# Kernel tuning notes

Hardware: AMD Instinct MI355X
Metric: run time of the kernel (lower is better)

Reference implementation:

```python
import jax, jax.numpy as jnp
import numpy as np


def _gru_dirs(x, h, w_ih, w_hh, b_ih, b_hh):
    # One GRU step for both directions at once (seq_len==1 per original loop).
    # x: [N, in], h: [2, N, H]; w_ih: [2, 3H, in], w_hh: [2, 3H, H], biases [2, 3H]
    gi = jnp.einsum('ni,dgi->dng', x, w_ih) + b_ih[:, None, :]
    gh = jnp.einsum('dnh,dgh->dng', h, w_hh) + b_hh[:, None, :]
    H = h.shape[-1]
    ir, iz, inn = gi[..., :H], gi[..., H:2 * H], gi[..., 2 * H:]
    hr, hz, hn = gh[..., :H], gh[..., H:2 * H], gh[..., 2 * H:]
    r = jax.nn.sigmoid(ir + hr)
    z = jax.nn.sigmoid(iz + hz)
    n = jnp.tanh(inn + r * hn)
    return (1.0 - z) * n + z * h


def setup_inputs() -> dict:
    key = jax.random.key(0)
    ks = jax.random.split(key, 6)
    V, E, H, NL = 32000, 1024, 512, 2  # vocab, input_size, hidden_size, num_layers
    N, L = 32, 512
    s = 0.05
    x = jax.random.randint(ks[0], (N, L), 0, V)
    emb = jax.random.normal(ks[1], (V, E), dtype=jnp.float32) * s
    w_ih = jax.random.normal(ks[2], (NL, 2, 3 * H, E), dtype=jnp.float32) * s
    w_hh = jax.random.normal(ks[3], (NL, 2, 3 * H, H), dtype=jnp.float32) * s
    b_ih = jax.random.normal(ks[4], (NL, 2, 3 * H), dtype=jnp.float32) * s
    b_hh = jax.random.normal(ks[5], (NL, 2, 3 * H), dtype=jnp.float32) * s
    return {"x": x, "emb": emb, "w_ih": w_ih, "w_hh": w_hh, "b_ih": b_ih, "b_hh": b_hh}


def reference(x, emb, w_ih, w_hh, b_ih, b_hh):
    # Because the torch code calls the bidirectional GRU one timestep at a time
    # with a carried hidden, BOTH directions scan left-to-right over the sequence.
    N, L = x.shape
    num_layers = w_ih.shape[0]
    H = w_hh.shape[-1]
    h0 = jnp.zeros((num_layers, 2, N, H), dtype=emb.dtype)

    def step(h, xt):
        layer_in = emb[xt]  # [N, E] embedding lookup for this timestep
        new_h = []
        for l in range(num_layers):  # fixed small layer loop
            hl = _gru_dirs(layer_in, h[l], w_ih[l], w_hh[l], b_ih[l], b_hh[l])
            new_h.append(hl)
            layer_in = jnp.concatenate([hl[0], hl[1]], axis=-1)  # [N, 2H]
        hs = jnp.stack(new_h)  # [num_layers, 2, N, H]
        return hs, (layer_in, hs)

    _, (outs, hiddens) = jax.lax.scan(step, h0, x.T)  # scan over L timesteps
    outputs = jnp.transpose(outs, (1, 0, 2))  # [N, L, 2H]
    hiddens = hiddens.reshape(L, num_layers * 2, N, H)  # [L, 2*num_layers, N, H]
    return outputs, hiddens
```

## Files before the change

### kernel.cpp

```cpp
#include <hip/hip_runtime.h>
#include <hip/hip_bf16.h>

using u16 = unsigned short;
using u32 = unsigned int;
using bf16x8 = __attribute__((ext_vector_type(8))) __bf16;
using f32x4  = __attribute__((ext_vector_type(4))) float;
using u32x4  = __attribute__((ext_vector_type(4))) u32;

#define GLP(p) ((const __attribute__((address_space(1))) void*)(p))
#define LDSP(p) ((__attribute__((address_space(3))) void*)(p))

__device__ __forceinline__ float bf2f(u16 u) {
    union { float f; u32 i; } v; v.i = ((u32)u) << 16; return v.f;
}
__device__ __forceinline__ u16 f2bf(float f) {
    union { float f; u32 i; } v; v.f = f;
    u32 r = v.i + 0x7FFFu + ((v.i >> 16) & 1u);
    return (u16)(r >> 16);
}

__device__ __forceinline__ u32 ld_sc01_u32(const u32* p) {
    u32 v;
    asm volatile("global_load_dword %0, %1, off sc0 sc1\n\ts_waitcnt vmcnt(0)"
                 : "=v"(v) : "v"(p) : "memory");
    return v;
}
__device__ __forceinline__ void st_sc01_u32(u32* p, u32 v) {
    asm volatile("global_store_dword %0, %1, off sc0 sc1" :: "v"(p), "v"(v) : "memory");
}
__device__ __forceinline__ void st_sc01_u16(u16* p, u16 v) {
    asm volatile("global_store_short %0, %1, off sc0 sc1" :: "v"(p), "v"(v) : "memory");
}
__device__ __forceinline__ void st_sc01_u32x4(u16* p, u32x4 v) {
    asm volatile("global_store_dwordx4 %0, %1, off sc0 sc1" :: "v"(p), "v"(v) : "memory");
}

__device__ __forceinline__ float sigm(float x) {
    return __builtin_amdgcn_rcpf(1.f + __expf(-x));
}
__device__ __forceinline__ float tanh_fast(float x) {
    float e = __expf(-2.f * x);
    return (1.f - e) * __builtin_amdgcn_rcpf(1.f + e);
}

__global__ void k_gather(const int* __restrict__ x, const float* __restrict__ emb,
                         u16* __restrict__ X0) {
    int gid = blockIdx.x * blockDim.x + threadIdx.x;
    if (gid >= 16384 * 256) return;
    int e4 = gid << 2;
    int m = e4 >> 10, k = e4 & 1023;
    int t = m >> 5, n = m & 31;
    int tok = x[n * 512 + t];
    float4 v = *reinterpret_cast<const float4*>(emb + ((size_t)tok << 10) + k);
    ushort4 o;
    o.x = f2bf(v.x); o.y = f2bf(v.y); o.z = f2bf(v.z); o.w = f2bf(v.w);
    *reinterpret_cast<ushort4*>(X0 + (size_t)e4) = o;
}

__global__ void k_f32bf16(const float* __restrict__ s, u16* __restrict__ d, int n4) {
    int gid = blockIdx.x * blockDim.x + threadIdx.x;
    if (gid >= n4) return;
    float4 v = reinterpret_cast<const float4*>(s)[gid];
    ushort4 o;
    o.x = f2bf(v.x); o.y = f2bf(v.y); o.z = f2bf(v.z); o.w = f2bf(v.w);
    reinterpret_cast<ushort4*>(d)[gid] = o;
}

template<int LAYER>
__device__ __forceinline__ void gru_body(char* smem, int d, int wg,
    const u16* __restrict__ Gi, const u16* __restrict__ Whh_l,
    const float* __restrict__ bhh_l, u16* __restrict__ hbuf,
    u16* __restrict__ X1, float* __restrict__ hid, float* __restrict__ outp,
    u32* __restrict__ flags, u32* __restrict__ xflags, const u32* __restrict__ gdone)
{
    char* hS          = smem;
    float (*ghs)[196] = (float(*)[196])(smem + 32768);
    u16 (*gis)[208]   = (u16(*)[208])(smem + 57856);
    float* bhh_s      = (float*)(smem + 71168);
    u16* hvS          = (u16*)(smem + 71936);
    volatile u32* rdy = (volatile u32*)(smem + 76032);
    const int tid = threadIdx.x;
    const int lane = tid & 63, w = tid >> 6;
    const int j0 = wg * 64;
    const int g = w >> 2;
    const int lr = lane & 15, lk = lane >> 4;

    if (tid < 192) {
        int g2 = tid >> 6, jj = tid & 63;
        bhh_s[tid] = bhh_l[d * 1536 + g2 * 512 + j0 + jj];
    }
    if (tid < 8) rdy[tid] = 0;
    bf16x8 wf[16];
    {
        const int joff = (w & 3) * 16;
        const u16* wr = Whh_l + (size_t)(d * 1536 + g * 512 + j0 + joff + lr) * 512 + lk * 8;
        #pragma unroll
        for (int kt = 0; kt < 16; ++kt)
            wf[kt] = *reinterpret_cast<const bf16x8*>(wr + kt * 32);
    }
    __syncthreads();

    u32* myflag = flags + (d * 8 + wg) * 32;
    const u32* wflag = flags + (d * 8 + (w & 7)) * 32;

    const int c8 = (lane & 7) * 8;
    const int rb = lane >> 3;
    const int colu = w * 64 + c8;
    const int ci0 = (tid - 512) * 3;

    float hpv[4] = {0.f, 0.f, 0.f, 0.f};
    u32 g_seen = 0;

    for (int t = 0; t < 512; ++t) {
        if (w < 8) {
            if (t > 0) {
                long long tt0 = __builtin_amdgcn_s_memrealtime();
                int k = 0;
                while (ld_sc01_u32(wflag) < (u32)t) {
                    if (++k >= 16) {
                        k = 0;
                        if (__builtin_amdgcn_s_memrealtime() - tt0 > 2000) {
                            if (lane == 0)
                                __hip_atomic_store(myflag, (u32)t, __ATOMIC_RELEASE,
                                                   __HIP_MEMORY_SCOPE_AGENT);
                            tt0 = __builtin_amdgcn_s_memrealtime();
                        }
                    }
                }
            }
            const u16* hb = hbuf + ((size_t)d * 2 + ((t + 1) & 1)) * 16384;
            u32x4 v0, v1, v2, v3;
            asm volatile("global_load_dwordx4 %0, %1, off sc0 sc1"
                         : "=v"(v0) : "v"(hb + (size_t)(rb)      * 512 + colu));
            asm volatile("global_load_dwordx4 %0, %1, off sc0 sc1"
                         : "=v"(v1) : "v"(hb + (size_t)(rb + 8)  * 512 + colu));
            asm volatile("global_load_dwordx4 %0, %1, off sc0 sc1"
                         : "=v"(v2) : "v"(hb + (size_t)(rb + 16) * 512 + colu));
            asm volatile("global_load_dwordx4 %0, %1, off sc0 sc1"
                         : "=v"(v3) : "v"(hb + (size_t)(rb + 24) * 512 + colu));
            asm volatile("s_waitcnt vmcnt(0)" ::: "memory");
            const int cb = colu * 2;
            *reinterpret_cast<u32x4*>(hS + (rb)      * 1024 + (cb ^ (((rb)      & 15) << 4))) = v0;
            *reinterpret_cast<u32x4*>(hS + (rb + 8)  * 1024 + (cb ^ (((rb + 8)  & 15) << 4))) = v1;
            *reinterpret_cast<u32x4*>(hS + (rb + 16) * 1024 + (cb ^ (((rb + 16) & 15) << 4))) = v2;
            *reinterpret_cast<u32x4*>(hS + (rb + 24) * 1024 + (cb ^ (((rb + 24) & 15) << 4))) = v3;
            asm volatile("s_waitcnt lgkmcnt(0)" ::: "memory");
            __builtin_amdgcn_sched_barrier(0);
            if (lane == 0) rdy[w] = (u32)(t + 1);
        } else {
            u32 yneed = (u32)(t >> 2);
            if (g_seen <= yneed) {
                const u32* gp = gdone + yneed;
                long long T0 = __builtin_amdgcn_s_memrealtime();
                while (ld_sc01_u32(gp) == 0) {
                    __builtin_amdgcn_s_sleep(1);
                    if (__builtin_amdgcn_s_memrealtime() - T0 > 2000000) break;
                }
                g_seen = yneed + 1;
            }
            u32x4 gq[3];
            int nbs[3], gcs[3];
            #pragma unroll
            for (int i = 0; i < 3; ++i) {
                int ci = ci0 + i;
                nbs[i] = ci / 24; gcs[i] = ci % 24;
                const u16* gp = Gi + (size_t)(t * 32 + nbs[i]) * 3072 + d * 1536
                              + (gcs[i] >> 3) * 512 + j0 + (gcs[i] & 7) * 8;
                asm volatile("global_load_dwordx4 %0, %1, off sc0 sc1"
                             : "=v"(gq[i]) : "v"(gp));
            }
            asm volatile("s_waitcnt vmcnt(0)" ::: "memory");
            #pragma unroll
            for (int i = 0; i < 3; ++i)
                *reinterpret_cast<u32x4*>(&gis[nbs[i]][gcs[i] * 8]) = gq[i];
        }

        f32x4 acc0 = {0.f, 0.f, 0.f, 0.f}, acc1 = acc0;
        #pragma unroll
        for (int s = 0; s < 8; ++s) {
            while (rdy[s] < (u32)(t + 1)) {}
            __builtin_amdgcn_sched_barrier(0);
            int b0 = (lk * 16 + (2 * s) * 64) ^ (lr << 4);
            int b1 = (lk * 16 + (2 * s + 1) * 64) ^ (lr << 4);
            bf16x8 a00 = *reinterpret_cast<const bf16x8*>(hS + lr * 1024 + b0);
            bf16x8 a10 = *reinterpret_cast<const bf16x8*>(hS + (16 + lr) * 1024 + b0);
            bf16x8 a01 = *reinterpret_cast<const bf16x8*>(hS + lr * 1024 + b1);
            bf16x8 a11 = *reinterpret_cast<const bf16x8*>(hS + (16 + lr) * 1024 + b1);
            acc0 = __builtin_amdgcn_mfma_f32_16x16x32_bf16(a00, wf[2 * s],     acc0, 0, 0, 0);
            acc1 = __builtin_amdgcn_mfma_f32_16x16x32_bf16(a10, wf[2 * s],     acc1, 0, 0, 0);
            acc0 = __builtin_amdgcn_mfma_f32_16x16x32_bf16(a01, wf[2 * s + 1], acc0, 0, 0, 0);
            acc1 = __builtin_amdgcn_mfma_f32_16x16x32_bf16(a11, wf[2 * s + 1], acc1, 0, 0, 0);
        }
        int colg = w * 16 + lr;
        float bv = bhh_s[colg];
        #pragma unroll
        for (int q = 0; q < 4; ++q) {
            ghs[lk * 4 + q][colg]      = acc0[q] + bv;
            ghs[16 + lk * 4 + q][colg] = acc1[q] + bv;
        }
        __syncthreads();

        u16* hbw = hbuf + ((size_t)d * 2 + (t & 1)) * 16384;
        #pragma unroll
        for (int rep = 0; rep < 2; ++rep) {
            int e2 = tid + rep * 768;
            if (e2 < 1024) {
                int jp = (e2 & 31) * 2, nb = e2 >> 5;
                float r0 = sigm(bf2f(gis[nb][jp])      + ghs[nb][jp]);
                float r1 = sigm(bf2f(gis[nb][jp + 1])  + ghs[nb][jp + 1]);
                float z0 = sigm(bf2f(gis[nb][64 + jp])     + ghs[nb][64 + jp]);
                float z1 = sigm(bf2f(gis[nb][64 + jp + 1]) + ghs[nb][64 + jp + 1]);
                float n0 = tanh_fast(bf2f(gis[nb][128 + jp])     + r0 * ghs[nb][128 + jp]);
                float n1 = tanh_fast(bf2f(gis[nb][128 + jp + 1]) + r1 * ghs[nb][128 + jp + 1]);
                float hv0 = (1.f - z0) * n0 + z0 * hpv[rep * 2];
                float hv1 = (1.f - z1) * n1 + z1 * hpv[rep * 2 + 1];
                hpv[rep * 2] = hv0; hpv[rep * 2 + 1] = hv1;
                u32 packed = (u32)f2bf(hv0) | ((u32)f2bf(hv1) << 16);
                st_sc01_u32((u32*)(hbw + (size_t)nb * 512 + j0 + jp), packed);
                *reinterpret_cast<u32*>(hvS + nb * 64 + jp) = packed;
            }
        }
        asm volatile("s_waitcnt vmcnt(0)" ::: "memory");
        __syncthreads();
        if (tid == 16)
            st_sc01_u32(myflag, (u32)(t + 1));

        if (tid >= 512) {
            int q = tid - 512, nb = q >> 3, j8 = (q & 7) * 8;
            union { u32x4 v; u16 s[8]; } h8;
            h8.v = *reinterpret_cast<const u32x4*>(hvS + nb * 64 + j8);
            float f0 = bf2f(h8.s[0]), f1 = bf2f(h8.s[1]), f2 = bf2f(h8.s[2]), f3 = bf2f(h8.s[3]);
            float f4 = bf2f(h8.s[4]), f5 = bf2f(h8.s[5]), f6 = bf2f(h8.s[6]), f7 = bf2f(h8.s[7]);
            float* hp = hid + ((size_t)(t * 4 + LAYER * 2 + d) * 32 + nb) * 512 + j0 + j8;
            *reinterpret_cast<float4*>(hp)     = make_float4(f0, f1, f2, f3);
            *reinterpret_cast<float4*>(hp + 4) = make_float4(f4, f5, f6, f7);
            if (LAYER == 0) {
                u16* xp = X1 + (size_t)(t * 32 + nb) * 1024 + (size_t)d * 512 + j0 + j8;
                st_sc01_u32x4(xp, h8.v);
            } else {
                float* op = outp + ((size_t)nb * 512 + t) * 1024 + (size_t)d * 512 + j0 + j8;
                *reinterpret_cast<float4*>(op)     = make_float4(f0, f1, f2, f3);
                *reinterpret_cast<float4*>(op + 4) = make_float4(f4, f5, f6, f7);
            }
        }
        if (LAYER == 0 && (t & 3) == 3) {
            asm volatile("s_waitcnt vmcnt(0)" ::: "memory");
            __syncthreads();
            if (tid == 17)
                st_sc01_u32(xflags + (d * 8 + wg) * 32, (u32)(t + 1));
        }
    }
}

__device__ __forceinline__ void chaser_body(char* smem, int cw,
    const u16* __restrict__ A, const u16* __restrict__ B,
    const float* __restrict__ bias, u16* __restrict__ Gi,
    const u32* __restrict__ xflags, u32* __restrict__ cnt, u32* __restrict__ done)
{
    u16* As = (u16*)smem;
    u16* Bs = (u16*)(smem + 16384);
    const int tid = threadIdx.x;
    const int lane = tid & 63, wid = tid >> 6;
    const int wm = wid & 1, wn = wid >> 1;
    const int lr = lane & 15, lk = lane >> 4;

    for (int T = cw; T < 4096; T += 48) {
        const int y = T >> 5, x = T & 31;
        if (xflags && tid < 16) {
            const u32* fp = xflags + tid * 32;
            u32 target = 4u * (u32)y + 4u;
            long long T0 = __builtin_amdgcn_s_memrealtime();
            while (ld_sc01_u32(fp) < target) {
                __builtin_amdgcn_s_sleep(4);
                if (__builtin_amdgcn_s_memrealtime() - T0 > 2000000) break;
            }
        }
        __syncthreads();

        f32x4 zero = {0.f, 0.f, 0.f, 0.f};
        f32x4 acc[4][2];
        #pragma unroll
        for (int i = 0; i < 4; ++i) { acc[i][0] = zero; acc[i][1] = zero; }

        for (int k0 = 0; k0 < 1024; k0 += 64) {
            #pragma unroll
            for (int r = 0; r < 5; ++r) {
                int c = wid * 5 + r;
                if (c < 16) {
                    int o = c * 1024 + lane * 16;
                    int row = o >> 7, kb = o & 127;
                    int kbs = kb ^ ((row & 7) << 4);
                    const char* s = (const char*)A + ((size_t)(y * 128 + row) * 1024 + k0) * 2 + kbs;
                    __builtin_amdgcn_global_load_lds(GLP(s), LDSP((char*)As + c * 1024), 16, 0, 0);
                } else if (c < 28) {
                    int c2 = c - 16;
                    int o = c2 * 1024 + lane * 16;
                    int row = o >> 7, kb = o & 127;
                    int kbs = kb ^ ((row & 7) << 4);
                    const char* s = (const char*)B + ((size_t)(x * 96 + row) * 1024 + k0) * 2 + kbs;
                    __builtin_amdgcn_global_load_lds(GLP(s), LDSP((char*)Bs + c2 * 1024), 16, 0, 0);
                }
            }
            __syncthreads();
            if (wid < 6) {
                #pragma unroll
                for (int kk = 0; kk < 2; ++kk) {
                    bf16x8 af[4], bfr[2];
                    int kb = kk * 64 + lk * 16;
                    #pragma unroll
                    for (int i = 0; i < 4; ++i) {
                        int rowA = wm * 64 + i * 16 + lr;
                        af[i] = *reinterpret_cast<const bf16x8*>((const char*)As + rowA * 128 + (kb ^ ((rowA & 7) << 4)));
                    }
                    #pragma unroll
                    for (int j = 0; j < 2; ++j) {
                        int rowB = wn * 32 + j * 16 + lr;
                        bfr[j] = *reinterpret_cast<const bf16x8*>((const char*)Bs + rowB * 128 + (kb ^ ((rowB & 7) << 4)));
                    }
                    #pragma unroll
                    for (int i = 0; i < 4; ++i)
                        #pragma unroll
                        for (int j = 0; j < 2; ++j)
                            acc[i][j] = __builtin_amdgcn_mfma_f32_16x16x32_bf16(af[i], bfr[j], acc[i][j], 0, 0, 0);
                }
            }
            __syncthreads();
        }
        if (wid < 6) {
            #pragma unroll
            for (int j = 0; j < 2; ++j) {
                int col = x * 96 + wn * 32 + j * 16 + lr;
                float bv = bias[col];
                #pragma unroll
                for (int i = 0; i < 4; ++i) {
                    int rowb = y * 128 + wm * 64 + i * 16 + lk * 4;
                    #pragma unroll
                    for (int q = 0; q < 4; ++q)
                        st_sc01_u16(Gi + (size_t)(rowb + q) * 3072 + col, f2bf(acc[i][j][q] + bv));
                }
            }
        }
        asm volatile("s_waitcnt vmcnt(0)" ::: "memory");
        __syncthreads();
        if (tid == 0) {
            u32 old = __hip_atomic_fetch_add(&cnt[y], 1u, __ATOMIC_RELAXED,
                                             __HIP_MEMORY_SCOPE_AGENT);
            if (old == 31u)
                st_sc01_u32((u32*)&done[y], 1u);
        }
    }
}

__global__ __launch_bounds__(768, 2) void k_fused(
    u16* __restrict__ Gi,
    const u16* __restrict__ X0, const u16* __restrict__ Wih,
    const float* __restrict__ b_ih,
    const u16* __restrict__ Whh, const float* __restrict__ bhh,
    u16* __restrict__ hbuf0, u16* __restrict__ hbuf1,
    u16* __restrict__ X1,
    float* __restrict__ hid, float* __restrict__ outp,
    u32* __restrict__ flags0, u32* __restrict__ flags1,
    u32* __restrict__ xflags,
    u32* __restrict__ g0cnt, u32* __restrict__ g0done,
    u32* __restrict__ g1cnt, u32* __restrict__ g1done)
{
    __shared__ __align__(16) char smem[76096];
    int bid = blockIdx.x;
    if (bid < 16) {
        gru_body<0>(smem, bid >> 3, bid & 7, Gi, Whh, bhh, hbuf0,
                    X1, hid, outp, flags0, xflags, g0done);
    } else if (bid < 64) {
        chaser_body(smem, bid - 16, X0, Wih, b_ih, Gi, nullptr, g0cnt, g0done);
    } else if (bid < 112) {
        chaser_body(smem, bid - 64, X1, Wih + (size_t)3072 * 1024, b_ih + 3072,
                    Gi, xflags, g1cnt, g1done);
    } else {
        int b = bid - 112;
        gru_body<1>(smem, b >> 3, b & 7, Gi, Whh + (size_t)3072 * 512, bhh + 3072,
                    hbuf1, nullptr, hid, outp, flags1, nullptr, g1done);
    }
}

extern "C" void kernel_launch(void* const* d_in, const int* in_sizes, int n_in,
                              void* d_out, int out_size, void* d_ws, size_t ws_size,
                              hipStream_t stream) {
    const int*   x    = (const int*)d_in[0];
    const float* emb  = (const float*)d_in[1];
    const float* w_ih = (const float*)d_in[2];
    const float* w_hh = (const float*)d_in[3];
    const float* b_ih = (const float*)d_in[4];
    const float* b_hh = (const float*)d_in[5];
    float* outp = (float*)d_out;
    float* hid  = outp + (size_t)32 * 512 * 1024;

    char* ws = (char*)d_ws;
    u16* X0     = (u16*)(ws);
    u16* X1     = (u16*)(ws + 33554432);
    u16* Wih    = (u16*)(ws + 67108864);
    u16* Whh    = (u16*)(ws + 79691776);
    u16* Gi     = (u16*)(ws + 85983232);
    u16* hbuf0  = (u16*)(ws + 186646528);
    u16* hbuf1  = (u16*)(ws + 186777600);
    u32* flags0 = (u32*)(ws + 186908672);
    u32* flags1 = (u32*)(ws + 186910720);
    u32* xflags = (u32*)(ws + 186912768);
    u32* g0cnt  = (u32*)(ws + 186914816);
    u32* g0done = (u32*)(ws + 186915328);
    u32* g1cnt  = (u32*)(ws + 186915840);
    u32* g1done = (u32*)(ws + 186916352);

    k_gather<<<16384, 256, 0, stream>>>(x, emb, X0);
    k_f32bf16<<<(1572864 + 255) / 256, 256, 0, stream>>>(w_ih, Wih, 1572864);
    k_f32bf16<<<( 786432 + 255) / 256, 256, 0, stream>>>(w_hh, Whh, 786432);

    (void)hipMemsetAsync(hbuf0, 0, 270336, stream);

    k_fused<<<128, 768, 0, stream>>>(Gi, X0, Wih, b_ih, Whh, b_hh,
                                     hbuf0, hbuf1, X1, hid, outp,
                                     flags0, flags1, xflags,
                                     g0cnt, g0done, g1cnt, g1done);
}
```

Measured before the change: 2.322 ms.

## Replace per-step flag handshake with timestep-tagged hidden-state words polled directly

Each hidden-state element is now stored as a 32-bit word with the timestep in its high half, so consumer workgroups poll the hidden buffer itself until every tag matches instead of spinning on separate per-workgroup flags and then loading. This removes the flag store, the store drain (vmcnt wait plus barrier) before signalling, and the LDS ready counters, replacing them with a single block barrier before the MFMA loop. Outputs, hiddens and X1 are written straight from the gate threads, which drops the hvS staging pass. The cost is twice the hidden-buffer traffic, repeated reloads while polling, and reliance on a dwordx2 store being seen atomically per element.

```diff
diff --git a/kernel.cpp b/kernel.cpp
--- a/kernel.cpp
+++ b/kernel.cpp
@@ -5,6 +5,7 @@
 using u32 = unsigned int;
 using bf16x8 = __attribute__((ext_vector_type(8))) __bf16;
 using f32x4  = __attribute__((ext_vector_type(4))) float;
+using u32x2  = __attribute__((ext_vector_type(2))) u32;
 using u32x4  = __attribute__((ext_vector_type(4))) u32;
 
 #define GLP(p) ((const __attribute__((address_space(1))) void*)(p))
@@ -28,11 +29,11 @@
 __device__ __forceinline__ void st_sc01_u32(u32* p, u32 v) {
     asm volatile("global_store_dword %0, %1, off sc0 sc1" :: "v"(p), "v"(v) : "memory");
 }
+__device__ __forceinline__ void st_sc01_u32x2(u32* p, u32x2 v) {
+    asm volatile("global_store_dwordx2 %0, %1, off sc0 sc1" :: "v"(p), "v"(v) : "memory");
+}
 __device__ __forceinline__ void st_sc01_u16(u16* p, u16 v) {
     asm volatile("global_store_short %0, %1, off sc0 sc1" :: "v"(p), "v"(v) : "memory");
-}
-__device__ __forceinline__ void st_sc01_u32x4(u16* p, u32x4 v) {
-    asm volatile("global_store_dwordx4 %0, %1, off sc0 sc1" :: "v"(p), "v"(v) : "memory");
 }
 
 __device__ __forceinline__ float sigm(float x) {
@@ -69,16 +70,14 @@
 template<int LAYER>
 __device__ __forceinline__ void gru_body(char* smem, int d, int wg,
     const u16* __restrict__ Gi, const u16* __restrict__ Whh_l,
-    const float* __restrict__ bhh_l, u16* __restrict__ hbuf,
+    const float* __restrict__ bhh_l, u32* __restrict__ hbuf,
     u16* __restrict__ X1, float* __restrict__ hid, float* __restrict__ outp,
-    u32* __restrict__ flags, u32* __restrict__ xflags, const u32* __restrict__ gdone)
+    u32* __restrict__ xflags, const u32* __restrict__ gdone)
 {
     char* hS          = smem;
     float (*ghs)[196] = (float(*)[196])(smem + 32768);
     u16 (*gis)[208]   = (u16(*)[208])(smem + 57856);
     float* bhh_s      = (float*)(smem + 71168);
-    u16* hvS          = (u16*)(smem + 71936);
-    volatile u32* rdy = (volatile u32*)(smem + 76032);
     const int tid = threadIdx.x;
     const int lane = tid & 63, w = tid >> 6;
     const int j0 = wg * 64;
@@ -89,7 +88,6 @@
         int g2 = tid >> 6, jj = tid & 63;
         bhh_s[tid] = bhh_l[d * 1536 + g2 * 512 + j0 + jj];
     }
-    if (tid < 8) rdy[tid] = 0;
     bf16x8 wf[16];
     {
         const int joff = (w & 3) * 16;
@@ -100,12 +98,9 @@
     }
     __syncthreads();
 
-    u32* myflag = flags + (d * 8 + wg) * 32;
-    const u32* wflag = flags + (d * 8 + (w & 7)) * 32;
-
-    const int c8 = (lane & 7) * 8;
+    const int colu = w * 64 + (lane & 7) * 8;
     const int rb = lane >> 3;
-    const int colu = w * 64 + c8;
+    const int cb = colu * 2;
     const int ci0 = (tid - 512) * 3;
 
     float hpv[4] = {0.f, 0.f, 0.f, 0.f};
@@ -113,40 +108,50 @@
 
     for (int t = 0; t < 512; ++t) {
         if (w < 8) {
-            if (t > 0) {
-                long long tt0 = __builtin_amdgcn_s_memrealtime();
-                int k = 0;
-                while (ld_sc01_u32(wflag) < (u32)t) {
-                    if (++k >= 16) {
-                        k = 0;
-                        if (__builtin_amdgcn_s_memrealtime() - tt0 > 2000) {
-                            if (lane == 0)
-                                __hip_atomic_store(myflag, (u32)t, __ATOMIC_RELEASE,
-                                                   __HIP_MEMORY_SCOPE_AGENT);
-                            tt0 = __builtin_amdgcn_s_memrealtime();
+            const u32* hb = hbuf + ((size_t)d * 2 + ((t + 1) & 1)) * 16384;
+            const u32 expt = (u32)t << 16;
+            u32x4 va[4][2];
+            bool fresh[4] = {false, false, false, false};
+            long long T0 = __builtin_amdgcn_s_memrealtime();
+            for (;;) {
+                #pragma unroll
+                for (int c = 0; c < 4; ++c) {
+                    if (!fresh[c]) {
+                        const u32* p = hb + (size_t)(rb + c * 8) * 512 + colu;
+                        asm volatile("global_load_dwordx4 %0, %1, off sc0 sc1"
+                                     : "=v"(va[c][0]) : "v"(p));
+                        asm volatile("global_load_dwordx4 %0, %1, off sc0 sc1"
+                                     : "=v"(va[c][1]) : "v"(p + 4));
+                    }
+                }
+                asm volatile("s_waitcnt vmcnt(0)" ::: "memory");
+                bool all4 = true;
+                #pragma unroll
+                for (int c = 0; c < 4; ++c) {
+                    if (!fresh[c]) {
+                        u32 xv = 0;
+                        #pragma unroll
+                        for (int i = 0; i < 4; ++i) {
+                            xv |= (va[c][0][i] ^ expt);
+                            xv |= (va[c][1][i] ^ expt);
                         }
+                        fresh[c] = ((xv & 0xFFFF0000u) == 0);
                     }
-                }
-            }
-            const u16* hb = hbuf + ((size_t)d * 2 + ((t + 1) & 1)) * 16384;
-            u32x4 v0, v1, v2, v3;
-            asm volatile("global_load_dwordx4 %0, %1, off sc0 sc1"
-                         : "=v"(v0) : "v"(hb + (size_t)(rb)      * 512 + colu));
-            asm volatile("global_load_dwordx4 %0, %1, off sc0 sc1"
-                         : "=v"(v1) : "v"(hb + (size_t)(rb + 8)  * 512 + colu));
-            asm volatile("global_load_dwordx4 %0, %1, off sc0 sc1"
-                         : "=v"(v2) : "v"(hb + (size_t)(rb + 16) * 512 + colu));
-            asm volatile("global_load_dwordx4 %0, %1, off sc0 sc1"
-                         : "=v"(v3) : "v"(hb + (size_t)(rb + 24) * 512 + colu));
-            asm volatile("s_waitcnt vmcnt(0)" ::: "memory");
-            const int cb = colu * 2;
-            *reinterpret_cast<u32x4*>(hS + (rb)      * 1024 + (cb ^ (((rb)      & 15) << 4))) = v0;
-            *reinterpret_cast<u32x4*>(hS + (rb + 8)  * 1024 + (cb ^ (((rb + 8)  & 15) << 4))) = v1;
-            *reinterpret_cast<u32x4*>(hS + (rb + 16) * 1024 + (cb ^ (((rb + 16) & 15) << 4))) = v2;
-            *reinterpret_cast<u32x4*>(hS + (rb + 24) * 1024 + (cb ^ (((rb + 24) & 15) << 4))) = v3;
-            asm volatile("s_waitcnt lgkmcnt(0)" ::: "memory");
-            __builtin_amdgcn_sched_barrier(0);
-            if (lane == 0) rdy[w] = (u32)(t + 1);
+                    all4 = all4 && fresh[c];
+                }
+                if (__all(all4)) break;
+                if (__builtin_amdgcn_s_memrealtime() - T0 > 2000000) break;
+            }
+            #pragma unroll
+            for (int c = 0; c < 4; ++c) {
+                int row = rb + c * 8;
+                u32x4 pk;
+                pk[0] = (va[c][0][0] & 0xFFFFu) | (va[c][0][1] << 16);
+                pk[1] = (va[c][0][2] & 0xFFFFu) | (va[c][0][3] << 16);
+                pk[2] = (va[c][1][0] & 0xFFFFu) | (va[c][1][1] << 16);
+                pk[3] = (va[c][1][2] & 0xFFFFu) | (va[c][1][3] << 16);
+                *reinterpret_cast<u32x4*>(hS + row * 1024 + (cb ^ ((row & 15) << 4))) = pk;
+            }
         } else {
             u32 yneed = (u32)(t >> 2);
             if (g_seen <= yneed) {
@@ -174,22 +179,16 @@
             for (int i = 0; i < 3; ++i)
                 *reinterpret_cast<u32x4*>(&gis[nbs[i]][gcs[i] * 8]) = gq[i];
         }
+        __syncthreads();
 
         f32x4 acc0 = {0.f, 0.f, 0.f, 0.f}, acc1 = acc0;
         #pragma unroll
-        for (int s = 0; s < 8; ++s) {
-            while (rdy[s] < (u32)(t + 1)) {}
-            __builtin_amdgcn_sched_barrier(0);
-            int b0 = (lk * 16 + (2 * s) * 64) ^ (lr << 4);
-            int b1 = (lk * 16 + (2 * s + 1) * 64) ^ (lr << 4);
-            bf16x8 a00 = *reinterpret_cast<const bf16x8*>(hS + lr * 1024 + b0);
-            bf16x8 a10 = *reinterpret_cast<const bf16x8*>(hS + (16 + lr) * 1024 + b0);
-            bf16x8 a01 = *reinterpret_cast<const bf16x8*>(hS + lr * 1024 + b1);
-            bf16x8 a11 = *reinterpret_cast<const bf16x8*>(hS + (16 + lr) * 1024 + b1);
-            acc0 = __builtin_amdgcn_mfma_f32_16x16x32_bf16(a00, wf[2 * s],     acc0, 0, 0, 0);
-            acc1 = __builtin_amdgcn_mfma_f32_16x16x32_bf16(a10, wf[2 * s],     acc1, 0, 0, 0);
-            acc0 = __builtin_amdgcn_mfma_f32_16x16x32_bf16(a01, wf[2 * s + 1], acc0, 0, 0, 0);
-            acc1 = __builtin_amdgcn_mfma_f32_16x16x32_bf16(a11, wf[2 * s + 1], acc1, 0, 0, 0);
+        for (int kt = 0; kt < 16; ++kt) {
+            int boff = (lk * 16 + kt * 64) ^ (lr << 4);
+            bf16x8 a0 = *reinterpret_cast<const bf16x8*>(hS + lr * 1024 + boff);
+            bf16x8 a1 = *reinterpret_cast<const bf16x8*>(hS + (16 + lr) * 1024 + boff);
+            acc0 = __builtin_amdgcn_mfma_f32_16x16x32_bf16(a0, wf[kt], acc0, 0, 0, 0);
+            acc1 = __builtin_amdgcn_mfma_f32_16x16x32_bf16(a1, wf[kt], acc1, 0, 0, 0);
         }
         int colg = w * 16 + lr;
         float bv = bhh_s[colg];
@@ -200,47 +199,36 @@
         }
         __syncthreads();
 
-        u16* hbw = hbuf + ((size_t)d * 2 + (t & 1)) * 16384;
+        u32* hbw = hbuf + ((size_t)d * 2 + (t & 1)) * 16384;
+        const u32 tagn = (u32)(t + 1) << 16;
         #pragma unroll
         for (int rep = 0; rep < 2; ++rep) {
-            int e2 = tid + rep * 768;
-            if (e2 < 1024) {
+            int e2 = (rep == 0) ? tid : tid + 256;
+            if (rep == 0 || tid >= 512) {
                 int jp = (e2 & 31) * 2, nb = e2 >> 5;
-                float r0 = sigm(bf2f(gis[nb][jp])      + ghs[nb][jp]);
-                float r1 = sigm(bf2f(gis[nb][jp + 1])  + ghs[nb][jp + 1]);
+                int rr = rep * 2;
+                float r0 = sigm(bf2f(gis[nb][jp])          + ghs[nb][jp]);
+                float r1 = sigm(bf2f(gis[nb][jp + 1])      + ghs[nb][jp + 1]);
                 float z0 = sigm(bf2f(gis[nb][64 + jp])     + ghs[nb][64 + jp]);
                 float z1 = sigm(bf2f(gis[nb][64 + jp + 1]) + ghs[nb][64 + jp + 1]);
                 float n0 = tanh_fast(bf2f(gis[nb][128 + jp])     + r0 * ghs[nb][128 + jp]);
                 float n1 = tanh_fast(bf2f(gis[nb][128 + jp + 1]) + r1 * ghs[nb][128 + jp + 1]);
-                float hv0 = (1.f - z0) * n0 + z0 * hpv[rep * 2];
-                float hv1 = (1.f - z1) * n1 + z1 * hpv[rep * 2 + 1];
-                hpv[rep * 2] = hv0; hpv[rep * 2 + 1] = hv1;
-                u32 packed = (u32)f2bf(hv0) | ((u32)f2bf(hv1) << 16);
-                st_sc01_u32((u32*)(hbw + (size_t)nb * 512 + j0 + jp), packed);
-                *reinterpret_cast<u32*>(hvS + nb * 64 + jp) = packed;
-            }
-        }
-        asm volatile("s_waitcnt vmcnt(0)" ::: "memory");
-        __syncthreads();
-        if (tid == 16)
-            st_sc01_u32(myflag, (u32)(t + 1));
-
-        if (tid >= 512) {
-            int q = tid - 512, nb = q >> 3, j8 = (q & 7) * 8;
-            union { u32x4 v; u16 s[8]; } h8;
-            h8.v = *reinterpret_cast<const u32x4*>(hvS + nb * 64 + j8);
-            float f0 = bf2f(h8.s[0]), f1 = bf2f(h8.s[1]), f2 = bf2f(h8.s[2]), f3 = bf2f(h8.s[3]);
-            float f4 = bf2f(h8.s[4]), f5 = bf2f(h8.s[5]), f6 = bf2f(h8.s[6]), f7 = bf2f(h8.s[7]);
-            float* hp = hid + ((size_t)(t * 4 + LAYER * 2 + d) * 32 + nb) * 512 + j0 + j8;
-            *reinterpret_cast<float4*>(hp)     = make_float4(f0, f1, f2, f3);
-            *reinterpret_cast<float4*>(hp + 4) = make_float4(f4, f5, f6, f7);
-            if (LAYER == 0) {
-                u16* xp = X1 + (size_t)(t * 32 + nb) * 1024 + (size_t)d * 512 + j0 + j8;
-                st_sc01_u32x4(xp, h8.v);
-            } else {
-                float* op = outp + ((size_t)nb * 512 + t) * 1024 + (size_t)d * 512 + j0 + j8;
-                *reinterpret_cast<float4*>(op)     = make_float4(f0, f1, f2, f3);
-                *reinterpret_cast<float4*>(op + 4) = make_float4(f4, f5, f6, f7);
+                float hv0 = (1.f - z0) * n0 + z0 * hpv[rr];
+                float hv1 = (1.f - z1) * n1 + z1 * hpv[rr + 1];
+                hpv[rr] = hv0; hpv[rr + 1] = hv1;
+                u16 b0 = f2bf(hv0), b1 = f2bf(hv1);
+                u32x2 pp = { (u32)b0 | tagn, (u32)b1 | tagn };
+                st_sc01_u32x2(hbw + (size_t)nb * 512 + j0 + jp, pp);
+                float2 hf; hf.x = hv0; hf.y = hv1;
+                *reinterpret_cast<float2*>(hid + ((size_t)(t * 4 + LAYER * 2 + d) * 32 + nb) * 512
+                                           + j0 + jp) = hf;
+                if (LAYER == 0) {
+                    st_sc01_u32((u32*)(X1 + (size_t)(t * 32 + nb) * 1024 + (size_t)d * 512 + j0 + jp),
+                                (u32)b0 | ((u32)b1 << 16));
+                } else {
+                    *reinterpret_cast<float2*>(outp + ((size_t)nb * 512 + t) * 1024
+                                               + (size_t)d * 512 + j0 + jp) = hf;
+                }
             }
         }
         if (LAYER == 0 && (t & 3) == 3) {
@@ -248,6 +236,10 @@
             __syncthreads();
             if (tid == 17)
                 st_sc01_u32(xflags + (d * 8 + wg) * 32, (u32)(t + 1));
+        } else {
+            __builtin_amdgcn_sched_barrier(0);
+            __builtin_amdgcn_s_barrier();
+            __builtin_amdgcn_sched_barrier(0);
         }
     }
 }
@@ -351,24 +343,23 @@
     }
 }
 
-__global__ __launch_bounds__(768, 2) void k_fused(
+__global__ __launch_bounds__(768, 3) void k_fused(
     u16* __restrict__ Gi,
     const u16* __restrict__ X0, const u16* __restrict__ Wih,
     const float* __restrict__ b_ih,
     const u16* __restrict__ Whh, const float* __restrict__ bhh,
-    u16* __restrict__ hbuf0, u16* __restrict__ hbuf1,
+    u32* __restrict__ hbuf0, u32* __restrict__ hbuf1,
     u16* __restrict__ X1,
     float* __restrict__ hid, float* __restrict__ outp,
-    u32* __restrict__ flags0, u32* __restrict__ flags1,
     u32* __restrict__ xflags,
     u32* __restrict__ g0cnt, u32* __restrict__ g0done,
     u32* __restrict__ g1cnt, u32* __restrict__ g1done)
 {
-    __shared__ __align__(16) char smem[76096];
+    __shared__ __align__(16) char smem[71936];
     int bid = blockIdx.x;
     if (bid < 16) {
         gru_body<0>(smem, bid >> 3, bid & 7, Gi, Whh, bhh, hbuf0,
-                    X1, hid, outp, flags0, xflags, g0done);
+                    X1, hid, outp, xflags, g0done);
     } else if (bid < 64) {
         chaser_body(smem, bid - 16, X0, Wih, b_ih, Gi, nullptr, g0cnt, g0done);
     } else if (bid < 112) {
@@ -377,7 +368,7 @@
     } else {
         int b = bid - 112;
         gru_body<1>(smem, b >> 3, b & 7, Gi, Whh + (size_t)3072 * 512, bhh + 3072,
-                    hbuf1, nullptr, hid, outp, flags1, nullptr, g1done);
+                    hbuf1, nullptr, hid, outp, nullptr, g1done);
     }
 }
 
@@ -399,24 +390,21 @@
     u16* Wih    = (u16*)(ws + 67108864);
     u16* Whh    = (u16*)(ws + 79691776);
     u16* Gi     = (u16*)(ws + 85983232);
-    u16* hbuf0  = (u16*)(ws + 186646528);
-    u16* hbuf1  = (u16*)(ws + 186777600);
-    u32* flags0 = (u32*)(ws + 186908672);
-    u32* flags1 = (u32*)(ws + 186910720);
-    u32* xflags = (u32*)(ws + 186912768);
-    u32* g0cnt  = (u32*)(ws + 186914816);
-    u32* g0done = (u32*)(ws + 186915328);
-    u32* g1cnt  = (u32*)(ws + 186915840);
-    u32* g1done = (u32*)(ws + 186916352);
+    u32* hbuf0  = (u32*)(ws + 186646528);
+    u32* hbuf1  = (u32*)(ws + 186908672);
+    u32* xflags = (u32*)(ws + 187170816);
+    u32* g0cnt  = (u32*)(ws + 187172864);
+    u32* g0done = (u32*)(ws + 187173376);
+    u32* g1cnt  = (u32*)(ws + 187173888);
+    u32* g1done = (u32*)(ws + 187174400);
 
     k_gather<<<16384, 256, 0, stream>>>(x, emb, X0);
     k_f32bf16<<<(1572864 + 255) / 256, 256, 0, stream>>>(w_ih, Wih, 1572864);
     k_f32bf16<<<( 786432 + 255) / 256, 256, 0, stream>>>(w_hh, Whh, 786432);
 
-    (void)hipMemsetAsync(hbuf0, 0, 270336, stream);
+    (void)hipMemsetAsync(hbuf0, 0, 528384, stream);
 
     k_fused<<<128, 768, 0, stream>>>(Gi, X0, Wih, b_ih, Whh, b_hh,
                                      hbuf0, hbuf1, X1, hid, outp,
-                                     flags0, flags1, xflags,
-                                     g0cnt, g0done, g1cnt, g1done);
-}
+                                     xflags, g0cnt, g0done, g1cnt, g1done);
+}
```

Measured after the change: 2.370 ms. 1.02x slower.
